# Performance work log

Hardware: AMD Instinct MI355X
Metric: run time of the kernel (lower is better)

## Reference

```python
import jax, jax.numpy as jnp
import numpy as np
from jax.ops import segment_sum

N, E, D, P, F_IN, L, G = 40000, 320000, 128, 16, 64, 3, 40


def setup_inputs():
    key = jax.random.key(0)
    ks = iter(jax.random.split(key, 64))
    nrm = lambda shape, s=0.1: s * jax.random.normal(next(ks), shape, jnp.float32)
    inp = {
        "node_feat": nrm((N, F_IN), 1.0),
        "pos_enc": nrm((N, P), 1.0),
        "edge_feat": nrm((E, 1), 1.0),
        "snorm_n": jnp.full((N, 1), 1.0 / np.sqrt(N / G), jnp.float32),
        "edge_src": jax.random.randint(next(ks), (E,), 0, N, jnp.int32),
        "edge_dst": jax.random.randint(next(ks), (E,), 0, N, jnp.int32),
        "batch_num_nodes": jnp.full((G,), N // G, jnp.int32),
        "W_h": nrm((F_IN, D)), "b_h": jnp.zeros((D,), jnp.float32),
        "W_p": nrm((P, D)), "b_p": jnp.zeros((D,), jnp.float32),
        "W_e": nrm((1, D)), "b_e": jnp.zeros((D,), jnp.float32),
        "A1_W": nrm((L, 2 * D, D)), "A1_b": jnp.zeros((L, D), jnp.float32),
        "A2_W": nrm((L, 2 * D, D)), "A2_b": jnp.zeros((L, D), jnp.float32),
        "B1_W": nrm((L, D, D)), "B1_b": jnp.zeros((L, D), jnp.float32),
        "B2_W": nrm((L, D, D)), "B2_b": jnp.zeros((L, D), jnp.float32),
        "B3_W": nrm((L, D, D)), "B3_b": jnp.zeros((L, D), jnp.float32),
        "C1_W": nrm((L, D, D)), "C1_b": jnp.zeros((L, D), jnp.float32),
        "C2_W": nrm((L, D, D)), "C2_b": jnp.zeros((L, D), jnp.float32),
        "bn_h_g": jnp.ones((L, D), jnp.float32), "bn_h_b": jnp.zeros((L, D), jnp.float32),
        "bn_e_g": jnp.ones((L, D), jnp.float32), "bn_e_b": jnp.zeros((L, D), jnp.float32),
        "pout_W": nrm((D, P)), "pout_b": jnp.zeros((P,), jnp.float32),
        "Whp_W": nrm((D + P, D)), "Whp_b": jnp.zeros((D,), jnp.float32),
        "mlp_W0": nrm((D, D // 2)), "mlp_b0": jnp.zeros((D // 2,), jnp.float32),
        "mlp_W1": nrm((D // 2, D // 4)), "mlp_b1": jnp.zeros((D // 4,), jnp.float32),
        "mlp_W2": nrm((D // 4, 1)), "mlp_b2": jnp.zeros((1,), jnp.float32),
    }
    return inp


def _bn(x, g, b, eps=1e-5):
    # BatchNorm1d with batch statistics (training-mode math, eval dropout)
    m = x.mean(0)
    v = x.var(0)
    return g * (x - m) / jnp.sqrt(v + eps) + b


def _forward(fl, edge_src, edge_dst, batch_num_nodes):
    n = fl["node_feat"].shape[0]
    h = fl["node_feat"] @ fl["W_h"] + fl["b_h"]
    p = fl["pos_enc"] @ fl["W_p"] + fl["b_p"]
    e = fl["edge_feat"] @ fl["W_e"] + fl["b_e"]
    snorm = fl["snorm_n"]
    for l in range(L):
        h_in, p_in, e_in = h, p, e
        hp_cat = jnp.concatenate([h, p], -1)                      # [N, 2D]
        A1h = hp_cat @ fl["A1_W"][l] + fl["A1_b"][l]
        A2h = hp_cat @ fl["A2_W"][l] + fl["A2_b"][l]
        B1h = h @ fl["B1_W"][l] + fl["B1_b"][l]
        B2h = h @ fl["B2_W"][l] + fl["B2_b"][l]
        B3e = e @ fl["B3_W"][l] + fl["B3_b"][l]
        hat_eta = B1h[edge_src] + B2h[edge_dst] + B3e             # [E, D]
        sigma = jax.nn.sigmoid(hat_eta)
        ssum = segment_sum(sigma, edge_dst, num_segments=n)       # [N, D]
        eta = sigma / (ssum[edge_dst] + 1e-6)                     # [E, D]
        h_new = A1h + segment_sum(eta * A2h[edge_src], edge_dst, num_segments=n)
        C1p = p @ fl["C1_W"][l] + fl["C1_b"][l]
        C2p = p @ fl["C2_W"][l] + fl["C2_b"][l]
        p_new = C1p + segment_sum(eta * C2p[edge_src], edge_dst, num_segments=n)
        h2 = jax.nn.relu(_bn(h_new * snorm, fl["bn_h_g"][l], fl["bn_h_b"][l]))
        e2 = jax.nn.relu(_bn(hat_eta, fl["bn_e_g"][l], fl["bn_e_b"][l]))
        p2 = jnp.tanh(p_new)
        h, p, e = h_in + h2, p_in + p2, e_in + e2                 # residual
    # LSPE readout: per-graph center and per-feature L2-normalize p
    p = p @ fl["pout_W"] + fl["pout_b"]                           # [N, P]
    gid = jnp.repeat(jnp.arange(G), batch_num_nodes, total_repeat_length=n)
    cnt = batch_num_nodes.astype(p.dtype)[:, None]
    p = p - (segment_sum(p, gid, num_segments=G) / cnt)[gid]
    p = p / jnp.sqrt(segment_sum(p * p, gid, num_segments=G))[gid]
    hp = jnp.concatenate([h, p], -1) @ fl["Whp_W"] + fl["Whp_b"]
    first_idx = jnp.concatenate([jnp.zeros((1,), jnp.int32),
                                 jnp.cumsum(batch_num_nodes)[:-1].astype(jnp.int32)])
    hg = hp[first_idx]                                            # [G, D]
    y = jax.nn.relu(hg @ fl["mlp_W0"] + fl["mlp_b0"])
    y = jax.nn.relu(y @ fl["mlp_W1"] + fl["mlp_b1"])
    return y @ fl["mlp_W2"] + fl["mlp_b2"]                        # [G, 1]


def reference(node_feat, pos_enc, edge_feat, snorm_n, edge_src, edge_dst,
              batch_num_nodes, W_h, b_h, W_p, b_p, W_e, b_e,
              A1_W, A1_b, A2_W, A2_b, B1_W, B1_b, B2_W, B2_b, B3_W, B3_b,
              C1_W, C1_b, C2_W, C2_b, bn_h_g, bn_h_b, bn_e_g, bn_e_b,
              pout_W, pout_b, Whp_W, Whp_b,
              mlp_W0, mlp_b0, mlp_W1, mlp_b1, mlp_W2, mlp_b2):
    args = dict(locals())
    src = args.pop("edge_src")
    dst = args.pop("edge_dst")
    bnn = args.pop("batch_num_nodes")
    return _forward(args, src, dst, bnn)
```

## Files before the change

### kernel.cpp

```cpp
#include <hip/hip_runtime.h>

#define NN 40000
#define NNP 40064
#define NE 320000
#define DD 128
#define PP 16
#define FIN 64
#define NL 3
#define NG 40

typedef float4 f4;
typedef __attribute__((ext_vector_type(4))) float f32x4;
typedef _Float16 hf;
typedef __attribute__((ext_vector_type(4))) _Float16 h4;
typedef __attribute__((ext_vector_type(8))) _Float16 h8;

__device__ hf    g_e   [NE * DD];
__device__ hf    g_heta[NE * DD];
__device__ float g_h   [NNP * DD], g_p [NNP * DD];
__device__ hf    g_h16 [NNP * DD], g_pf [NNP * DD];
__device__ float g_A1h [NNP * DD], g_C1p[NNP * DD];
__device__ hf    g_A2h [NNP * DD], g_B1h[NNP * DD], g_B2h[NNP * DD], g_C2p[NNP * DD];
__device__ float g_st  [768];
__device__ float g_p16 [NN * PP], g_psum[NG * PP], g_pss[NG * PP];
__device__ int   g_cum [64];
__device__ int   g_deg[NN], g_rowptr[NN + 1], g_cursor[NN], g_perm[NE], g_ssrc[NE], g_sdst[NE];
__device__ hf    g_WA[2 * NL * DD * 256];
__device__ hf    g_WB[5 * NL * DD * DD];

__device__ __forceinline__ float sigm(float x) { return 1.0f / (1.0f + __expf(-x)); }

__global__ void k_zero(float* __restrict__ p, int n4)
{
    int i = blockIdx.x * 256 + threadIdx.x;
    if (i < n4) ((f4*)p)[i] = f4{0.f, 0.f, 0.f, 0.f};
}

__global__ void k_zeroi(int* __restrict__ p, int n)
{
    int i = blockIdx.x * 256 + threadIdx.x;
    if (i < n) p[i] = 0;
}

__global__ void k_deg(const int* __restrict__ dst, int* __restrict__ deg)
{
    int e = blockIdx.x * 256 + threadIdx.x;
    if (e < NE) atomicAdd(&deg[dst[e]], 1);
}

__global__ __launch_bounds__(1024)
void k_scan(const int* __restrict__ deg, int* __restrict__ rowptr, int* __restrict__ cursor)
{
    __shared__ int sums[1024];
    int t = threadIdx.x;
    const int chunk = (NN + 1023) / 1024;
    int base = t * chunk;
    int s = 0;
    for (int i = 0; i < chunk; ++i) { int idx = base + i; if (idx < NN) s += deg[idx]; }
    sums[t] = s;
    __syncthreads();
    for (int off = 1; off < 1024; off <<= 1) {
        int v = (t >= off) ? sums[t - off] : 0;
        __syncthreads();
        sums[t] += v;
        __syncthreads();
    }
    int run = (t == 0) ? 0 : sums[t - 1];
    for (int i = 0; i < chunk; ++i) {
        int idx = base + i;
        if (idx < NN) { rowptr[idx] = run; cursor[idx] = run; run += deg[idx]; }
    }
    if (t == 1023) rowptr[NN] = sums[1023];
}

__global__ void k_fill(const int* __restrict__ dst, int* __restrict__ cursor,
                       int* __restrict__ perm)
{
    int e = blockIdx.x * 256 + threadIdx.x;
    if (e < NE) {
        int pos = atomicAdd(&cursor[dst[e]], 1);
        perm[pos] = e;
    }
}

__global__ void k_sortidx(const int* __restrict__ perm, const int* __restrict__ src,
                          const int* __restrict__ dst, int* __restrict__ ssrc,
                          int* __restrict__ sdst)
{
    int i = blockIdx.x * 256 + threadIdx.x;
    if (i < NE) { int e = perm[i]; ssrc[i] = src[e]; sdst[i] = dst[e]; }
}

__global__ void k_wprepA(const float* __restrict__ A1W, const float* __restrict__ A2W,
                         hf* __restrict__ outh)
{
    int which = blockIdx.z, l = blockIdx.y;
    int idx = blockIdx.x * 256 + threadIdx.x;
    int k = idx >> 7, n = idx & 127;
    const float* W = (which == 0 ? A1W : A2W) + (size_t)l * 256 * 128;
    outh[((size_t)which * NL + l) * DD * 256 + (size_t)n * 256 + k] = (hf)W[k * 128 + n];
}

__global__ void k_wprepB(const float* __restrict__ B1W, const float* __restrict__ B2W,
                         const float* __restrict__ B3W, const float* __restrict__ C1W,
                         const float* __restrict__ C2W, hf* __restrict__ outh)
{
    int which = blockIdx.z, l = blockIdx.y;
    int idx = blockIdx.x * 256 + threadIdx.x;
    int k = idx >> 7, n = idx & 127;
    const float* W;
    switch (which) { case 0: W = B1W; break; case 1: W = B2W; break;
                     case 2: W = B3W; break; case 3: W = C1W; break; default: W = C2W; }
    W += (size_t)l * 128 * 128;
    outh[((size_t)which * NL + l) * DD * DD + (size_t)n * 128 + k] = (hf)W[k * 128 + n];
}

template<int K>
__global__ __launch_bounds__(256)
void k_gemmF(const float* __restrict__ A, const float* __restrict__ W,
             const float* __restrict__ bias, float* __restrict__ C)
{
    __shared__ float As[64][20];
    __shared__ float Ws[16][128];
    const int tid = threadIdx.x;
    const int m0 = blockIdx.x * 64;
    const int ti = tid >> 4;
    const int tj = tid & 15;
    float acc[4][8];
    {
        float bv[8];
        #pragma unroll
        for (int c = 0; c < 8; ++c) bv[c] = bias[tj * 8 + c];
        #pragma unroll
        for (int r = 0; r < 4; ++r)
            #pragma unroll
            for (int c = 0; c < 8; ++c) acc[r][c] = bv[c];
    }
    const int ar = tid >> 2;
    const int ac = (tid & 3) * 4;
    for (int k0 = 0; k0 < K; k0 += 16) {
        f4 av = *(const f4*)(A + (size_t)(m0 + ar) * K + k0 + ac);
        *(f4*)&As[ar][ac] = av;
        {
            int q = tid;   int kr = q >> 5, c4 = (q & 31) * 4;
            *(f4*)&Ws[kr][c4] = *(const f4*)(W + (size_t)(k0 + kr) * 128 + c4);
            q = tid + 256; kr = q >> 5; c4 = (q & 31) * 4;
            *(f4*)&Ws[kr][c4] = *(const f4*)(W + (size_t)(k0 + kr) * 128 + c4);
        }
        __syncthreads();
        #pragma unroll
        for (int kk = 0; kk < 16; ++kk) {
            float a0 = As[ti * 4 + 0][kk];
            float a1 = As[ti * 4 + 1][kk];
            float a2 = As[ti * 4 + 2][kk];
            float a3 = As[ti * 4 + 3][kk];
            f4 w0 = *(f4*)&Ws[kk][tj * 8];
            f4 w1 = *(f4*)&Ws[kk][tj * 8 + 4];
            float wv[8] = {w0.x, w0.y, w0.z, w0.w, w1.x, w1.y, w1.z, w1.w};
            #pragma unroll
            for (int c = 0; c < 8; ++c) {
                acc[0][c] += a0 * wv[c];
                acc[1][c] += a1 * wv[c];
                acc[2][c] += a2 * wv[c];
                acc[3][c] += a3 * wv[c];
            }
        }
        __syncthreads();
    }
    #pragma unroll
    for (int r = 0; r < 4; ++r) {
        int row = m0 + ti * 4 + r;
        f4 o0 = {acc[r][0], acc[r][1], acc[r][2], acc[r][3]};
        f4 o1 = {acc[r][4], acc[r][5], acc[r][6], acc[r][7]};
        *(f4*)(C + (size_t)row * 128 + tj * 8)     = o0;
        *(f4*)(C + (size_t)row * 128 + tj * 8 + 4) = o1;
    }
}

struct NArgs {
    const hf* W[6];
    const float* bs[6];
    void* out[6];
};

__global__ __launch_bounds__(256)
void k_gemmN(NArgs a, const hf* __restrict__ hp, const hf* __restrict__ pp)
{
    __shared__ __align__(16) char smem[20480];
    hf (*As)[40] = (hf(*)[40])smem;
    hf (*Wh)[40] = (hf(*)[40])(smem + 10240);
    float* fstg = (float*)smem;
    hf*    hstg = (hf*)smem;
    const int tid = threadIdx.x;
    const int y = blockIdx.y;
    const int m0 = blockIdx.x * 128;
    const int K = (y < 2) ? 256 : 128;
    const hf* Wt = a.W[y];
    const int wid = tid >> 6, lane = tid & 63;
    const int lg = lane >> 4, ln = lane & 15;

    f32x4 acc[2][8];
    #pragma unroll
    for (int mt = 0; mt < 2; ++mt)
        #pragma unroll
        for (int nt = 0; nt < 8; ++nt) acc[mt][nt] = f32x4{0.f, 0.f, 0.f, 0.f};

    const int r1 = tid >> 2, g1 = (tid & 3) * 8;
    const int r2 = r1 + 64,  g2 = g1;

    for (int k0 = 0; k0 < K; k0 += 32) {
        const hf* pA; int kk;
        if (y < 2) {
            if (k0 >= 128) { pA = pp; kk = k0 - 128; }
            else           { pA = hp; kk = k0; }
        } else if (y < 4) { pA = hp; kk = k0; }
        else              { pA = pp; kk = k0; }
        *(f4*)&As[r1][g1] = *(const f4*)(pA + (size_t)(m0 + r1) * 128 + kk + g1);
        *(f4*)&As[r2][g2] = *(const f4*)(pA + (size_t)(m0 + r2) * 128 + kk + g2);
        *(f4*)&Wh[r1][g1] = *(const f4*)(Wt + (size_t)r1 * K + k0 + g1);
        *(f4*)&Wh[r2][g2] = *(const f4*)(Wt + (size_t)r2 * K + k0 + g2);
        __syncthreads();

        const int koff = lg * 8;
        h8 a0 = *(h8*)&As[wid * 32 + ln][koff];
        h8 a1 = *(h8*)&As[wid * 32 + 16 + ln][koff];
        #pragma unroll
        for (int nt = 0; nt < 8; ++nt) {
            h8 wh = *(h8*)&Wh[nt * 16 + ln][koff];
            acc[0][nt] = __builtin_amdgcn_mfma_f32_16x16x32_f16(a0, wh, acc[0][nt], 0, 0, 0);
            acc[1][nt] = __builtin_amdgcn_mfma_f32_16x16x32_f16(a1, wh, acc[1][nt], 0, 0, 0);
        }
        __syncthreads();
    }

    const float* bias = a.bs[y];
    const bool isF32 = (y == 0 || y == 4);
    if (isF32) {
        float* C = (float*)a.out[y];
        for (int pass = 0; pass < 4; ++pass) {
            if (wid == pass) {
                #pragma unroll
                for (int mt = 0; mt < 2; ++mt)
                    #pragma unroll
                    for (int nt = 0; nt < 8; ++nt)
                        #pragma unroll
                        for (int j = 0; j < 4; ++j)
                            fstg[(mt * 16 + lg * 4 + j) * 132 + nt * 16 + ln]
                                = acc[mt][nt][j] + bias[nt * 16 + ln];
            }
            __syncthreads();
            #pragma unroll
            for (int it = 0; it < 4; ++it) {
                int idx = it * 256 + tid;
                int r = idx >> 5, c4 = (idx & 31) * 4;
                *(f4*)(C + (size_t)(m0 + pass * 32 + r) * 128 + c4) = *(f4*)&fstg[r * 132 + c4];
            }
            __syncthreads();
        }
    } else {
        hf* C = (hf*)a.out[y];
        for (int pass = 0; pass < 4; ++pass) {
            if (wid == pass) {
                #pragma unroll
                for (int mt = 0; mt < 2; ++mt)
                    #pragma unroll
                    for (int nt = 0; nt < 8; ++nt)
                        #pragma unroll
                        for (int j = 0; j < 4; ++j)
                            hstg[(mt * 16 + lg * 4 + j) * 136 + nt * 16 + ln]
                                = (hf)(acc[mt][nt][j] + bias[nt * 16 + ln]);
            }
            __syncthreads();
            #pragma unroll
            for (int it = 0; it < 2; ++it) {
                int idx = it * 256 + tid;
                int r = idx >> 4, c8 = (idx & 15) * 8;
                *(f4*)(C + (size_t)(m0 + pass * 32 + r) * 128 + c8) = *(f4*)&hstg[r * 136 + c8];
            }
            __syncthreads();
        }
    }
}

template<bool EUPD, bool STATS>
__global__ __launch_bounds__(256)
void k_gemmE(hf* E, const hf* hetaPrev, hf* Cheta,
             const float* __restrict__ estPrev, const float* __restrict__ gamE,
             const float* __restrict__ betE,
             const hf* __restrict__ Wt,
             const float* __restrict__ bias,
             const hf* __restrict__ Gs, const hf* __restrict__ Gd,
             const int* __restrict__ srcI, const int* __restrict__ dstI,
             float* st, int wb)
{
    __shared__ __align__(16) char smem[20480];
    __shared__ float bnS[128], bnT[128];
    hf (*Ae)[40] = (hf(*)[40])smem;
    hf (*Wh)[40] = (hf(*)[40])(smem + 10240);
    float* sred = (float*)smem;
    hf*    hstg = (hf*)(smem + 1024);
    const int tid = threadIdx.x;
    const int m0 = blockIdx.x * 128;
    const int wid = tid >> 6, lane = tid & 63;
    const int lg = lane >> 4, ln = lane & 15;

    if (EUPD) {
        if (tid < 128) {
            const float invME = 1.0f / NE;
            float m = estPrev[tid] * invME;
            float v = estPrev[128 + tid] * invME - m * m;
            float inv = 1.0f / sqrtf(v + 1e-5f);
            float gg = gamE[tid];
            bnS[tid] = gg * inv;
            bnT[tid] = betE[tid] - gg * m * inv;
        }
        __syncthreads();
    }

    f32x4 acc[2][8];
    #pragma unroll
    for (int mt = 0; mt < 2; ++mt)
        #pragma unroll
        for (int nt = 0; nt < 8; ++nt) acc[mt][nt] = f32x4{0.f, 0.f, 0.f, 0.f};

    const int r1 = tid >> 2, g1 = (tid & 3) * 8;
    const int r2 = r1 + 64,  g2 = g1;

    for (int k0 = 0; k0 < 128; k0 += 32) {
        if (EUPD) {
            #pragma unroll
            for (int half = 0; half < 2; ++half) {
                int r = half ? r2 : r1;
                int g = half ? g2 : g1;
                int row = m0 + r, cb = k0 + g;
                h8 ev = *(const h8*)(E + (size_t)row * 128 + cb);
                h8 tv = *(const h8*)(hetaPrev + (size_t)row * 128 + cb);
                h8 nv;
                #pragma unroll
                for (int j = 0; j < 8; ++j) {
                    float xn = (float)tv[j] * bnS[cb + j] + bnT[cb + j];
                    float en = (float)ev[j] + fmaxf(xn, 0.f);
                    nv[j] = (hf)en;
                }
                *(h8*)&Ae[r][g] = nv;
                if (wb) *(h8*)(E + (size_t)row * 128 + cb) = nv;
            }
        } else {
            *(f4*)&Ae[r1][g1] = *(const f4*)(E + (size_t)(m0 + r1) * 128 + k0 + g1);
            *(f4*)&Ae[r2][g2] = *(const f4*)(E + (size_t)(m0 + r2) * 128 + k0 + g2);
        }
        *(f4*)&Wh[r1][g1] = *(const f4*)(Wt + (size_t)r1 * 128 + k0 + g1);
        *(f4*)&Wh[r2][g2] = *(const f4*)(Wt + (size_t)r2 * 128 + k0 + g2);
        __syncthreads();

        const int koff = lg * 8;
        h8 a0 = *(h8*)&Ae[wid * 32 + ln][koff];
        h8 a1 = *(h8*)&Ae[wid * 32 + 16 + ln][koff];
        #pragma unroll
        for (int nt = 0; nt < 8; ++nt) {
            h8 wh = *(h8*)&Wh[nt * 16 + ln][koff];
            acc[0][nt] = __builtin_amdgcn_mfma_f32_16x16x32_f16(a0, wh, acc[0][nt], 0, 0, 0);
            acc[1][nt] = __builtin_amdgcn_mfma_f32_16x16x32_f16(a1, wh, acc[1][nt], 0, 0, 0);
        }
        __syncthreads();
    }

    if (STATS) { sred[tid] = 0.f; __syncthreads(); }

    #pragma unroll
    for (int mt = 0; mt < 2; ++mt) {
        const int grow = m0 + wid * 32 + mt * 16 + lg * 4;
        int sa[4], da[4];
        #pragma unroll
        for (int j = 0; j < 4; ++j) { sa[j] = srcI[grow + j]; da[j] = dstI[grow + j]; }
        #pragma unroll
        for (int nt = 0; nt < 8; ++nt) {
            const int col = nt * 16 + ln;
            const float b = bias[col];
            float ls = 0.f, lq = 0.f;
            #pragma unroll
            for (int j = 0; j < 4; ++j) {
                float x = acc[mt][nt][j] + b
                        + (float)Gs[(size_t)sa[j] * 128 + col]
                        + (float)Gd[(size_t)da[j] * 128 + col];
                acc[mt][nt][j] = x;
                if (STATS) { ls += x; lq += x * x; }
            }
            if (STATS) {
                ls += __shfl_xor(ls, 16); ls += __shfl_xor(ls, 32);
                lq += __shfl_xor(lq, 16); lq += __shfl_xor(lq, 32);
                if (lane < 16) {
                    atomicAdd(&sred[col], ls);
                    atomicAdd(&sred[128 + col], lq);
                }
            }
        }
    }

    for (int pass = 0; pass < 4; ++pass) {
        if (wid == pass) {
            #pragma unroll
            for (int mt = 0; mt < 2; ++mt)
                #pragma unroll
                for (int nt = 0; nt < 8; ++nt)
                    #pragma unroll
                    for (int j = 0; j < 4; ++j)
                        hstg[(mt * 16 + lg * 4 + j) * 136 + nt * 16 + ln]
                            = (hf)acc[mt][nt][j];
        }
        __syncthreads();
        #pragma unroll
        for (int it = 0; it < 2; ++it) {
            int idx = it * 256 + tid;
            int r = idx >> 4, c8 = (idx & 15) * 8;
            *(f4*)(Cheta + (size_t)(m0 + pass * 32 + r) * 128 + c8) = *(f4*)&hstg[r * 136 + c8];
        }
        __syncthreads();
    }
    if (STATS) atomicAdd(&st[tid], sred[tid]);
}


__global__ void k_cvt16(const float* __restrict__ x, hf* __restrict__ y, int n4)
{
    int i = blockIdx.x * 256 + threadIdx.x;
    if (i >= n4) return;
    f4 v = ((const f4*)x)[i];
    ((h4*)y)[i] = h4{(hf)v.x, (hf)v.y, (hf)v.z, (hf)v.w};
}

__global__ void k_einit(const float* __restrict__ ef, const int* __restrict__ perm,
                        const float* __restrict__ We, const float* __restrict__ be,
                        hf* __restrict__ E)
{
    size_t id = (size_t)blockIdx.x * 256 + threadIdx.x;
    int row = (int)(id >> 5);
    int c = (int)(id & 31) * 4;
    float s = ef[perm[row]];
    f4 w = *(const f4*)(We + c);
    f4 b = *(const f4*)(be + c);
    *(h4*)(E + (size_t)row * 128 + c)
        = h4{(hf)(s * w.x + b.x), (hf)(s * w.y + b.y), (hf)(s * w.z + b.z), (hf)(s * w.w + b.w)};
}

__global__ void k_agg(const hf* __restrict__ heta, const hf* __restrict__ A2h,
                      const hf* __restrict__ C2p, const int* __restrict__ rowptr,
                      const int* __restrict__ ssrc, const float* __restrict__ snorm,
                      float* __restrict__ A1h, const float* __restrict__ C1p,
                      float* __restrict__ p, hf* __restrict__ pf,
                      float* __restrict__ st, int wp)
{
    size_t id = (size_t)blockIdx.x * 256 + threadIdx.x;
    int row = (int)(id >> 5);
    int c = (int)(id & 31) * 4;
    int s0 = rowptr[row], s1 = rowptr[row + 1];

    f4 ss = {0.f, 0.f, 0.f, 0.f};
    f4 ah = {0.f, 0.f, 0.f, 0.f};
    f4 cp = {0.f, 0.f, 0.f, 0.f};
    for (int e = s0; e < s1; ++e) {
        h4 v = *(const h4*)(heta + (size_t)e * 128 + c);
        int s = ssrc[e];
        h4 a = *(const h4*)(A2h + (size_t)s * 128 + c);
        h4 cc = *(const h4*)(C2p + (size_t)s * 128 + c);
        float g0 = sigm((float)v[0]), g1 = sigm((float)v[1]);
        float g2 = sigm((float)v[2]), g3 = sigm((float)v[3]);
        ss.x += g0; ss.y += g1; ss.z += g2; ss.w += g3;
        ah.x += g0 * (float)a[0]; ah.y += g1 * (float)a[1];
        ah.z += g2 * (float)a[2]; ah.w += g3 * (float)a[3];
        cp.x += g0 * (float)cc[0]; cp.y += g1 * (float)cc[1];
        cp.z += g2 * (float)cc[2]; cp.w += g3 * (float)cc[3];
    }
    ss.x += 1e-6f; ss.y += 1e-6f; ss.z += 1e-6f; ss.w += 1e-6f;
    ah.x /= ss.x; ah.y /= ss.y; ah.z /= ss.z; ah.w /= ss.w;
    cp.x /= ss.x; cp.y /= ss.y; cp.z /= ss.z; cp.w /= ss.w;

    float sn = snorm[row];
    f4 a1 = *(const f4*)(A1h + (size_t)row * 128 + c);
    f4 hx = {(a1.x + ah.x) * sn, (a1.y + ah.y) * sn, (a1.z + ah.z) * sn, (a1.w + ah.w) * sn};
    *(f4*)(A1h + (size_t)row * 128 + c) = hx;

    f4 c1 = *(const f4*)(C1p + (size_t)row * 128 + c);
    f4 pv = *(const f4*)(p + (size_t)row * 128 + c);
    pv.x += tanhf(c1.x + cp.x);
    pv.y += tanhf(c1.y + cp.y);
    pv.z += tanhf(c1.z + cp.z);
    pv.w += tanhf(c1.w + cp.w);
    *(f4*)(p + (size_t)row * 128 + c) = pv;
    if (wp)
        *(h4*)(pf + (size_t)row * 128 + c) = h4{(hf)pv.x, (hf)pv.y, (hf)pv.z, (hf)pv.w};

    __shared__ float red[8][128];
    int lrow = threadIdx.x >> 5;
    red[lrow][c + 0] = hx.x; red[lrow][c + 1] = hx.y;
    red[lrow][c + 2] = hx.z; red[lrow][c + 3] = hx.w;
    __syncthreads();
    if (threadIdx.x < 128) {
        float a = 0.f;
        #pragma unroll
        for (int q = 0; q < 8; ++q) a += red[q][threadIdx.x];
        atomicAdd(&st[threadIdx.x], a);
    }
    __syncthreads();
    red[lrow][c + 0] = hx.x * hx.x; red[lrow][c + 1] = hx.y * hx.y;
    red[lrow][c + 2] = hx.z * hx.z; red[lrow][c + 3] = hx.w * hx.w;
    __syncthreads();
    if (threadIdx.x < 128) {
        float a = 0.f;
        #pragma unroll
        for (int q = 0; q < 8; ++q) a += red[q][threadIdx.x];
        atomicAdd(&st[128 + threadIdx.x], a);
    }
}

__global__ void k_bnupd_h(float* __restrict__ Y, hf* __restrict__ Y16,
                          const float* __restrict__ X, const float* __restrict__ st,
                          const float* __restrict__ gam, const float* __restrict__ bet, float invM)
{
    size_t id = (size_t)blockIdx.x * 256 + threadIdx.x;
    int row = (int)(id >> 5);
    int c = (int)(id & 31) * 4;
    f4 x  = *(const f4*)(X + (size_t)row * 128 + c);
    f4 s  = *(const f4*)(st + c);
    f4 s2 = *(const f4*)(st + 128 + c);
    f4 g  = *(const f4*)(gam + c);
    f4 b  = *(const f4*)(bet + c);
    f4 y  = *(const f4*)(Y + (size_t)row * 128 + c);
    float m, v, o;
    m = s.x * invM; v = s2.x * invM - m * m; o = g.x * (x.x - m) / sqrtf(v + 1e-5f) + b.x; y.x += fmaxf(o, 0.f);
    m = s.y * invM; v = s2.y * invM - m * m; o = g.y * (x.y - m) / sqrtf(v + 1e-5f) + b.y; y.y += fmaxf(o, 0.f);
    m = s.z * invM; v = s2.z * invM - m * m; o = g.z * (x.z - m) / sqrtf(v + 1e-5f) + b.z; y.z += fmaxf(o, 0.f);
    m = s.w * invM; v = s2.w * invM - m * m; o = g.w * (x.w - m) / sqrtf(v + 1e-5f) + b.w; y.w += fmaxf(o, 0.f);
    *(f4*)(Y + (size_t)row * 128 + c) = y;
    *(h4*)(Y16 + (size_t)row * 128 + c) = h4{(hf)y.x, (hf)y.y, (hf)y.z, (hf)y.w};
}


__global__ void k_p16(const float* __restrict__ p, const float* __restrict__ poutW,
                      const float* __restrict__ poutb, float* __restrict__ p16)
{
    int id = blockIdx.x * 256 + threadIdx.x;
    int i = id >> 4, c = id & 15;
    float a = poutb[c];
    for (int k = 0; k < 128; ++k) a += p[(size_t)i * 128 + k] * poutW[k * 16 + c];
    p16[id] = a;
}

__global__ void k_cum(const int* __restrict__ bnn, int* __restrict__ cum)
{
    if (threadIdx.x == 0) {
        cum[0] = 0;
        for (int g = 0; g < NG; ++g) cum[g + 1] = cum[g] + bnn[g];
    }
}

__global__ void k_graphstats(const float* __restrict__ p16, const int* __restrict__ cum,
                             float* __restrict__ psum, float* __restrict__ pss)
{
    int g = blockIdx.x;
    int t = threadIdx.x;
    int c = t & 15, s = t >> 4;
    int start = cum[g], end = cum[g + 1];
    float cnt = (float)(end - start);
    __shared__ float red[16][17];
    __shared__ float meanv[16];
    float loc = 0.f;
    for (int i = start + s; i < end; i += 16) loc += p16[(size_t)i * 16 + c];
    red[s][c] = loc;
    __syncthreads();
    if (s == 0) {
        float a = 0.f;
        #pragma unroll
        for (int q = 0; q < 16; ++q) a += red[q][c];
        psum[g * 16 + c] = a;
        meanv[c] = a / cnt;
    }
    __syncthreads();
    float m = meanv[c];
    loc = 0.f;
    for (int i = start + s; i < end; i += 16) {
        float v = p16[(size_t)i * 16 + c] - m;
        loc += v * v;
    }
    red[s][c] = loc;
    __syncthreads();
    if (s == 0) {
        float a = 0.f;
        #pragma unroll
        for (int q = 0; q < 16; ++q) a += red[q][c];
        pss[g * 16 + c] = a;
    }
}

__global__ void k_final(const float* __restrict__ h, const float* __restrict__ A1h,
                        const float* __restrict__ hst, const float* __restrict__ gam,
                        const float* __restrict__ bet,
                        const float* __restrict__ p16,
                        const float* __restrict__ psum, const float* __restrict__ pss,
                        const int* __restrict__ cum,
                        const float* __restrict__ WhpW, const float* __restrict__ Whpb,
                        const float* __restrict__ W0, const float* __restrict__ b0,
                        const float* __restrict__ W1, const float* __restrict__ b1,
                        const float* __restrict__ W2, const float* __restrict__ b2,
                        float* __restrict__ out)
{
    int g = blockIdx.x;
    int t = threadIdx.x;
    __shared__ float hpc[144];
    __shared__ float hpv[128];
    __shared__ float y0[64];
    __shared__ float y1[32];
    int fi = cum[g];
    float cnt = (float)(cum[g + 1] - cum[g]);
    {
        const float invM = 1.0f / NN;
        float m = hst[t] * invM;
        float v = hst[128 + t] * invM - m * m;
        float x = A1h[(size_t)fi * 128 + t];
        float o = gam[t] * (x - m) / sqrtf(v + 1e-5f) + bet[t];
        hpc[t] = h[(size_t)fi * 128 + t] + fmaxf(o, 0.f);
    }
    if (t < 16) {
        float centered = p16[(size_t)fi * 16 + t] - psum[g * 16 + t] / cnt;
        hpc[128 + t] = centered / sqrtf(pss[g * 16 + t]);
    }
    __syncthreads();
    float acc = Whpb[t];
    for (int k = 0; k < 144; ++k) acc += hpc[k] * WhpW[k * 128 + t];
    hpv[t] = acc;
    __syncthreads();
    if (t < 64) {
        float a = b0[t];
        for (int k = 0; k < 128; ++k) a += hpv[k] * W0[k * 64 + t];
        y0[t] = fmaxf(a, 0.f);
    }
    __syncthreads();
    if (t < 32) {
        float a = b1[t];
        for (int k = 0; k < 64; ++k) a += y0[k] * W1[k * 32 + t];
        y1[t] = fmaxf(a, 0.f);
    }
    __syncthreads();
    if (t == 0) {
        float a = b2[0];
        for (int k = 0; k < 32; ++k) a += y1[k] * W2[k];
        out[g] = a;
    }
}


extern "C" void kernel_launch(void* const* d_in, const int* in_sizes, int n_in,
                              void* d_out, int out_size, void* d_ws, size_t ws_size,
                              hipStream_t stream)
{
    (void)in_sizes; (void)n_in; (void)out_size; (void)d_ws; (void)ws_size;
    const float* node_feat = (const float*)d_in[0];
    const float* pos_enc   = (const float*)d_in[1];
    const float* edge_feat = (const float*)d_in[2];
    const float* snorm     = (const float*)d_in[3];
    const int*   src       = (const int*)d_in[4];
    const int*   dst       = (const int*)d_in[5];
    const int*   bnn       = (const int*)d_in[6];
    const float* W_h = (const float*)d_in[7],  *b_h = (const float*)d_in[8];
    const float* W_p = (const float*)d_in[9],  *b_p = (const float*)d_in[10];
    const float* W_e = (const float*)d_in[11], *b_e = (const float*)d_in[12];
    const float* A1W = (const float*)d_in[13], *A1b = (const float*)d_in[14];
    const float* A2W = (const float*)d_in[15], *A2b = (const float*)d_in[16];
    const float* B1W = (const float*)d_in[17], *B1b = (const float*)d_in[18];
    const float* B2W = (const float*)d_in[19], *B2b = (const float*)d_in[20];
    const float* B3W = (const float*)d_in[21], *B3b = (const float*)d_in[22];
    const float* C1W = (const float*)d_in[23], *C1b = (const float*)d_in[24];
    const float* C2W = (const float*)d_in[25], *C2b = (const float*)d_in[26];
    const float* bnhg = (const float*)d_in[27], *bnhb = (const float*)d_in[28];
    const float* bneg = (const float*)d_in[29], *bneb = (const float*)d_in[30];
    const float* poutW = (const float*)d_in[31], *poutb = (const float*)d_in[32];
    const float* WhpW = (const float*)d_in[33], *Whpb = (const float*)d_in[34];
    const float* W0 = (const float*)d_in[35], *b0 = (const float*)d_in[36];
    const float* W1 = (const float*)d_in[37], *b1 = (const float*)d_in[38];
    const float* W2 = (const float*)d_in[39], *b2 = (const float*)d_in[40];
    float* out = (float*)d_out;

    float *h, *p, *A1h, *C1p, *st, *p16, *psum, *pss;
    hf *e, *heta, *h16, *pf, *A2h, *B1h, *B2h, *C2p, *WA, *WB;
    int *cum, *deg, *rowptr, *cursor, *perm, *ssrc, *sdst;
    hipGetSymbolAddress((void**)&e,      HIP_SYMBOL(g_e));
    hipGetSymbolAddress((void**)&heta,   HIP_SYMBOL(g_heta));
    hipGetSymbolAddress((void**)&h,      HIP_SYMBOL(g_h));
    hipGetSymbolAddress((void**)&p,      HIP_SYMBOL(g_p));
    hipGetSymbolAddress((void**)&h16,    HIP_SYMBOL(g_h16));
    hipGetSymbolAddress((void**)&pf,     HIP_SYMBOL(g_pf));
    hipGetSymbolAddress((void**)&A1h,    HIP_SYMBOL(g_A1h));
    hipGetSymbolAddress((void**)&C1p,    HIP_SYMBOL(g_C1p));
    hipGetSymbolAddress((void**)&A2h,    HIP_SYMBOL(g_A2h));
    hipGetSymbolAddress((void**)&B1h,    HIP_SYMBOL(g_B1h));
    hipGetSymbolAddress((void**)&B2h,    HIP_SYMBOL(g_B2h));
    hipGetSymbolAddress((void**)&C2p,    HIP_SYMBOL(g_C2p));
    hipGetSymbolAddress((void**)&st,     HIP_SYMBOL(g_st));
    hipGetSymbolAddress((void**)&p16,    HIP_SYMBOL(g_p16));
    hipGetSymbolAddress((void**)&psum,   HIP_SYMBOL(g_psum));
    hipGetSymbolAddress((void**)&pss,    HIP_SYMBOL(g_pss));
    hipGetSymbolAddress((void**)&cum,    HIP_SYMBOL(g_cum));
    hipGetSymbolAddress((void**)&deg,    HIP_SYMBOL(g_deg));
    hipGetSymbolAddress((void**)&rowptr, HIP_SYMBOL(g_rowptr));
    hipGetSymbolAddress((void**)&cursor, HIP_SYMBOL(g_cursor));
    hipGetSymbolAddress((void**)&perm,   HIP_SYMBOL(g_perm));
    hipGetSymbolAddress((void**)&ssrc,   HIP_SYMBOL(g_ssrc));
    hipGetSymbolAddress((void**)&sdst,   HIP_SYMBOL(g_sdst));
    hipGetSymbolAddress((void**)&WA,     HIP_SYMBOL(g_WA));
    hipGetSymbolAddress((void**)&WB,     HIP_SYMBOL(g_WB));
    float* hst  = st;
    float* estA = st + 256;
    float* estB = st + 512;

    k_zeroi<<<(NN + 255) / 256, 256, 0, stream>>>(deg, NN);
    k_deg<<<(NE + 255) / 256, 256, 0, stream>>>(dst, deg);
    k_scan<<<1, 1024, 0, stream>>>(deg, rowptr, cursor);
    k_fill<<<(NE + 255) / 256, 256, 0, stream>>>(dst, cursor, perm);
    k_sortidx<<<(NE + 255) / 256, 256, 0, stream>>>(perm, src, dst, ssrc, sdst);
    k_wprepA<<<dim3(128, NL, 2), 256, 0, stream>>>(A1W, A2W, WA);
    k_wprepB<<<dim3(64, NL, 5), 256, 0, stream>>>(B1W, B2W, B3W, C1W, C2W, WB);

    k_gemmF<FIN><<<NN / 64, 256, 0, stream>>>(node_feat, W_h, b_h, h);
    k_gemmF<PP ><<<NN / 64, 256, 0, stream>>>(pos_enc,  W_p, b_p, p);
    k_cvt16<<<(NNP * 32 + 255) / 256, 256, 0, stream>>>(h, h16, NNP * 32);
    k_cvt16<<<(NNP * 32 + 255) / 256, 256, 0, stream>>>(p, pf, NNP * 32);
    k_einit<<<NE * 32 / 256, 256, 0, stream>>>(edge_feat, perm, W_e, b_e, e);

    const int NB = NNP / 128;
    for (int l = 0; l < NL; ++l) {
        const hf* WB3 = WB + (size_t)(2 * NL + l) * DD * DD;

        NArgs na;
        na.W[0] = WA + (size_t)(0 * NL + l) * DD * 256;
        na.W[1] = WA + (size_t)(1 * NL + l) * DD * 256;
        na.W[2] = WB + (size_t)(0 * NL + l) * DD * DD;
        na.W[3] = WB + (size_t)(1 * NL + l) * DD * DD;
        na.W[4] = WB + (size_t)(3 * NL + l) * DD * DD;
        na.W[5] = WB + (size_t)(4 * NL + l) * DD * DD;
        na.bs[0] = A1b + l * DD; na.bs[1] = A2b + l * DD;
        na.bs[2] = B1b + l * DD; na.bs[3] = B2b + l * DD;
        na.bs[4] = C1b + l * DD; na.bs[5] = C2b + l * DD;
        na.out[0] = A1h; na.out[1] = A2h; na.out[2] = B1h;
        na.out[3] = B2h; na.out[4] = C1p; na.out[5] = C2p;
        k_gemmN<<<dim3(NB, 6), 256, 0, stream>>>(na, h16, pf);

        k_zero<<<1, 256, 0, stream>>>(hst, 64);

        if (l == 0) {
            k_zero<<<1, 256, 0, stream>>>(estA, 64);
            k_gemmE<false, true><<<NE / 128, 256, 0, stream>>>(
                e, nullptr, heta, nullptr, nullptr, nullptr,
                WB3, B3b + l * DD, B1h, B2h, ssrc, sdst, estA, 0);
        } else if (l == 1) {
            k_zero<<<1, 256, 0, stream>>>(estB, 64);
            k_gemmE<true, true><<<NE / 128, 256, 0, stream>>>(
                e, heta, heta, estA, bneg + 0 * DD, bneb + 0 * DD,
                WB3, B3b + l * DD, B1h, B2h, ssrc, sdst, estB, 1);
        } else {
            k_gemmE<true, false><<<NE / 128, 256, 0, stream>>>(
                e, heta, heta, estB, bneg + 1 * DD, bneb + 1 * DD,
                WB3, B3b + l * DD, B1h, B2h, ssrc, sdst, nullptr, 0);
        }

        k_agg<<<NN * 32 / 256, 256, 0, stream>>>(heta, A2h, C2p, rowptr, ssrc, snorm,
                                                 A1h, C1p, p, pf, hst,
                                                 (l < NL - 1) ? 1 : 0);

        if (l < NL - 1)
            k_bnupd_h<<<NN * 32 / 256, 256, 0, stream>>>(h, h16, A1h, hst,
                                                         bnhg + l * DD, bnhb + l * DD, 1.0f / NN);
    }

    k_p16<<<NN * 16 / 256, 256, 0, stream>>>(p, poutW, poutb, p16);
    k_cum<<<1, 64, 0, stream>>>(bnn, cum);
    k_graphstats<<<NG, 256, 0, stream>>>(p16, cum, psum, pss);
    k_final<<<NG, 128, 0, stream>>>(h, A1h, hst, bnhg + (NL - 1) * DD, bnhb + (NL - 1) * DD,
                                    p16, psum, pss, cum,
                                    WhpW, Whpb, W0, b0, W1, b1, W2, b2, out);
}
```

Baseline: 1.228 ms.

## Fold B1/B2 node projections into edge GEMM via concatenated gathered input

Removes the separate node-level B1/B2 GEMM outputs and instead has the edge GEMM multiply a K=384 concatenation of edge features, gathered h[src] and gathered h[dst] against stacked B3/B1/B2 weights, with summed biases. This eliminates writing and scattered element-wise gathering of B1h/B2h in the epilogue in favor of coalesced row gathers during the A-tile load. The trade-off is roughly tripling the edge GEMM's matrix work, recomputing projections per edge rather than per node.

```diff
diff --git a/kernel.cpp b/kernel.cpp
--- a/kernel.cpp
+++ b/kernel.cpp
@@ -20,13 +20,14 @@
 __device__ float g_h   [NNP * DD], g_p [NNP * DD];
 __device__ hf    g_h16 [NNP * DD], g_pf [NNP * DD];
 __device__ float g_A1h [NNP * DD], g_C1p[NNP * DD];
-__device__ hf    g_A2h [NNP * DD], g_B1h[NNP * DD], g_B2h[NNP * DD], g_C2p[NNP * DD];
-__device__ float g_st  [768];
+__device__ hf    g_A2h [NNP * DD], g_C2p[NNP * DD];
+__device__ float g_st  [896];
 __device__ float g_p16 [NN * PP], g_psum[NG * PP], g_pss[NG * PP];
 __device__ int   g_cum [64];
 __device__ int   g_deg[NN], g_rowptr[NN + 1], g_cursor[NN], g_perm[NE], g_ssrc[NE], g_sdst[NE];
 __device__ hf    g_WA[2 * NL * DD * 256];
-__device__ hf    g_WB[5 * NL * DD * DD];
+__device__ hf    g_WC[2 * NL * DD * DD];
+__device__ hf    g_WE[NL * DD * 384];
 
 __device__ __forceinline__ float sigm(float x) { return 1.0f / (1.0f + __expf(-x)); }
 
@@ -40,6 +41,13 @@
 {
     int i = blockIdx.x * 256 + threadIdx.x;
     if (i < n) p[i] = 0;
+}
+
+__global__ void k_ebias(const float* __restrict__ B1b, const float* __restrict__ B2b,
+                        const float* __restrict__ B3b, int l, float* __restrict__ outb)
+{
+    int t = threadIdx.x;
+    if (t < 128) outb[t] = B1b[l * 128 + t] + B2b[l * 128 + t] + B3b[l * 128 + t];
 }
 
 __global__ void k_deg(const int* __restrict__ dst, int* __restrict__ deg)
@@ -101,18 +109,29 @@
     outh[((size_t)which * NL + l) * DD * 256 + (size_t)n * 256 + k] = (hf)W[k * 128 + n];
 }
 
-__global__ void k_wprepB(const float* __restrict__ B1W, const float* __restrict__ B2W,
-                         const float* __restrict__ B3W, const float* __restrict__ C1W,
-                         const float* __restrict__ C2W, hf* __restrict__ outh)
+__global__ void k_wprepC(const float* __restrict__ C1W, const float* __restrict__ C2W,
+                         hf* __restrict__ outh)
 {
     int which = blockIdx.z, l = blockIdx.y;
     int idx = blockIdx.x * 256 + threadIdx.x;
     int k = idx >> 7, n = idx & 127;
+    const float* W = (which == 0 ? C1W : C2W) + (size_t)l * 128 * 128;
+    outh[((size_t)which * NL + l) * DD * DD + (size_t)n * 128 + k] = (hf)W[k * 128 + n];
+}
+
+__global__ void k_wprepE(const float* __restrict__ B1W, const float* __restrict__ B2W,
+                         const float* __restrict__ B3W, hf* __restrict__ outh)
+{
+    int l = blockIdx.y;
+    int idx = blockIdx.x * 256 + threadIdx.x;
+    int k = idx >> 7, n = idx & 127;
     const float* W;
-    switch (which) { case 0: W = B1W; break; case 1: W = B2W; break;
-                     case 2: W = B3W; break; case 3: W = C1W; break; default: W = C2W; }
+    int kk;
+    if (k < 128)      { W = B3W; kk = k; }
+    else if (k < 256) { W = B1W; kk = k - 128; }
+    else              { W = B2W; kk = k - 256; }
     W += (size_t)l * 128 * 128;
-    outh[((size_t)which * NL + l) * DD * DD + (size_t)n * 128 + k] = (hf)W[k * 128 + n];
+    outh[(size_t)l * DD * 384 + (size_t)n * 384 + k] = (hf)W[kk * 128 + n];
 }
 
 template<int K>
@@ -178,9 +197,9 @@
 }
 
 struct NArgs {
-    const hf* W[6];
-    const float* bs[6];
-    void* out[6];
+    const hf* W[4];
+    const float* bs[4];
+    void* out[4];
 };
 
 __global__ __launch_bounds__(256)
@@ -213,8 +232,7 @@
         if (y < 2) {
             if (k0 >= 128) { pA = pp; kk = k0 - 128; }
             else           { pA = hp; kk = k0; }
-        } else if (y < 4) { pA = hp; kk = k0; }
-        else              { pA = pp; kk = k0; }
+        } else { pA = pp; kk = k0; }
         *(f4*)&As[r1][g1] = *(const f4*)(pA + (size_t)(m0 + r1) * 128 + kk + g1);
         *(f4*)&As[r2][g2] = *(const f4*)(pA + (size_t)(m0 + r2) * 128 + kk + g2);
         *(f4*)&Wh[r1][g1] = *(const f4*)(Wt + (size_t)r1 * K + k0 + g1);
@@ -234,7 +252,7 @@
     }
 
     const float* bias = a.bs[y];
-    const bool isF32 = (y == 0 || y == 4);
+    const bool isF32 = (y == 0 || y == 2);
     if (isF32) {
         float* C = (float*)a.out[y];
         for (int pass = 0; pass < 4; ++pass) {
@@ -289,7 +307,7 @@
              const float* __restrict__ betE,
              const hf* __restrict__ Wt,
              const float* __restrict__ bias,
-             const hf* __restrict__ Gs, const hf* __restrict__ Gd,
+             const hf* __restrict__ h16,
              const int* __restrict__ srcI, const int* __restrict__ dstI,
              float* st, int wb)
 {
@@ -325,32 +343,44 @@
 
     const int r1 = tid >> 2, g1 = (tid & 3) * 8;
     const int r2 = r1 + 64,  g2 = g1;
-
-    for (int k0 = 0; k0 < 128; k0 += 32) {
-        if (EUPD) {
-            #pragma unroll
-            for (int half = 0; half < 2; ++half) {
-                int r = half ? r2 : r1;
-                int g = half ? g2 : g1;
-                int row = m0 + r, cb = k0 + g;
-                h8 ev = *(const h8*)(E + (size_t)row * 128 + cb);
-                h8 tv = *(const h8*)(hetaPrev + (size_t)row * 128 + cb);
-                h8 nv;
+    const int s1 = srcI[m0 + r1], s2 = srcI[m0 + r2];
+    const int d1 = dstI[m0 + r1], d2 = dstI[m0 + r2];
+
+    for (int k0 = 0; k0 < 384; k0 += 32) {
+        if (k0 < 128) {
+            if (EUPD) {
                 #pragma unroll
-                for (int j = 0; j < 8; ++j) {
-                    float xn = (float)tv[j] * bnS[cb + j] + bnT[cb + j];
-                    float en = (float)ev[j] + fmaxf(xn, 0.f);
-                    nv[j] = (hf)en;
+                for (int half = 0; half < 2; ++half) {
+                    int r = half ? r2 : r1;
+                    int g = half ? g2 : g1;
+                    int row = m0 + r, cb = k0 + g;
+                    h8 ev = *(const h8*)(E + (size_t)row * 128 + cb);
+                    h8 tv = *(const h8*)(hetaPrev + (size_t)row * 128 + cb);
+                    h8 nv;
+                    #pragma unroll
+                    for (int j = 0; j < 8; ++j) {
+                        float xn = (float)tv[j] * bnS[cb + j] + bnT[cb + j];
+                        float en = (float)ev[j] + fmaxf(xn, 0.f);
+                        nv[j] = (hf)en;
+                    }
+                    *(h8*)&Ae[r][g] = nv;
+                    if (wb) *(h8*)(E + (size_t)row * 128 + cb) = nv;
                 }
-                *(h8*)&Ae[r][g] = nv;
-                if (wb) *(h8*)(E + (size_t)row * 128 + cb) = nv;
+            } else {
+                *(f4*)&Ae[r1][g1] = *(const f4*)(E + (size_t)(m0 + r1) * 128 + k0 + g1);
+                *(f4*)&Ae[r2][g2] = *(const f4*)(E + (size_t)(m0 + r2) * 128 + k0 + g2);
             }
+        } else if (k0 < 256) {
+            int kk = k0 - 128;
+            *(f4*)&Ae[r1][g1] = *(const f4*)(h16 + (size_t)s1 * 128 + kk + g1);
+            *(f4*)&Ae[r2][g2] = *(const f4*)(h16 + (size_t)s2 * 128 + kk + g2);
         } else {
-            *(f4*)&Ae[r1][g1] = *(const f4*)(E + (size_t)(m0 + r1) * 128 + k0 + g1);
-            *(f4*)&Ae[r2][g2] = *(const f4*)(E + (size_t)(m0 + r2) * 128 + k0 + g2);
-        }
-        *(f4*)&Wh[r1][g1] = *(const f4*)(Wt + (size_t)r1 * 128 + k0 + g1);
-        *(f4*)&Wh[r2][g2] = *(const f4*)(Wt + (size_t)r2 * 128 + k0 + g2);
+            int kk = k0 - 256;
+            *(f4*)&Ae[r1][g1] = *(const f4*)(h16 + (size_t)d1 * 128 + kk + g1);
+            *(f4*)&Ae[r2][g2] = *(const f4*)(h16 + (size_t)d2 * 128 + kk + g2);
+        }
+        *(f4*)&Wh[r1][g1] = *(const f4*)(Wt + (size_t)r1 * 384 + k0 + g1);
+        *(f4*)&Wh[r2][g2] = *(const f4*)(Wt + (size_t)r2 * 384 + k0 + g2);
         __syncthreads();
 
         const int koff = lg * 8;
@@ -369,10 +399,6 @@
 
     #pragma unroll
     for (int mt = 0; mt < 2; ++mt) {
-        const int grow = m0 + wid * 32 + mt * 16 + lg * 4;
-        int sa[4], da[4];
-        #pragma unroll
-        for (int j = 0; j < 4; ++j) { sa[j] = srcI[grow + j]; da[j] = dstI[grow + j]; }
         #pragma unroll
         for (int nt = 0; nt < 8; ++nt) {
             const int col = nt * 16 + ln;
@@ -380,9 +406,7 @@
             float ls = 0.f, lq = 0.f;
             #pragma unroll
             for (int j = 0; j < 4; ++j) {
-                float x = acc[mt][nt][j] + b
-                        + (float)Gs[(size_t)sa[j] * 128 + col]
-                        + (float)Gd[(size_t)da[j] * 128 + col];
+                float x = acc[mt][nt][j] + b;
                 acc[mt][nt][j] = x;
                 if (STATS) { ls += x; lq += x * x; }
             }
@@ -681,7 +705,7 @@
     float* out = (float*)d_out;
 
     float *h, *p, *A1h, *C1p, *st, *p16, *psum, *pss;
-    hf *e, *heta, *h16, *pf, *A2h, *B1h, *B2h, *C2p, *WA, *WB;
+    hf *e, *heta, *h16, *pf, *A2h, *C2p, *WA, *WC, *WE;
     int *cum, *deg, *rowptr, *cursor, *perm, *ssrc, *sdst;
     hipGetSymbolAddress((void**)&e,      HIP_SYMBOL(g_e));
     hipGetSymbolAddress((void**)&heta,   HIP_SYMBOL(g_heta));
@@ -692,8 +716,6 @@
     hipGetSymbolAddress((void**)&A1h,    HIP_SYMBOL(g_A1h));
     hipGetSymbolAddress((void**)&C1p,    HIP_SYMBOL(g_C1p));
     hipGetSymbolAddress((void**)&A2h,    HIP_SYMBOL(g_A2h));
-    hipGetSymbolAddress((void**)&B1h,    HIP_SYMBOL(g_B1h));
-    hipGetSymbolAddress((void**)&B2h,    HIP_SYMBOL(g_B2h));
     hipGetSymbolAddress((void**)&C2p,    HIP_SYMBOL(g_C2p));
     hipGetSymbolAddress((void**)&st,     HIP_SYMBOL(g_st));
     hipGetSymbolAddress((void**)&p16,    HIP_SYMBOL(g_p16));
@@ -707,10 +729,12 @@
     hipGetSymbolAddress((void**)&ssrc,   HIP_SYMBOL(g_ssrc));
     hipGetSymbolAddress((void**)&sdst,   HIP_SYMBOL(g_sdst));
     hipGetSymbolAddress((void**)&WA,     HIP_SYMBOL(g_WA));
-    hipGetSymbolAddress((void**)&WB,     HIP_SYMBOL(g_WB));
-    float* hst  = st;
-    float* estA = st + 256;
-    float* estB = st + 512;
+    hipGetSymbolAddress((void**)&WC,     HIP_SYMBOL(g_WC));
+    hipGetSymbolAddress((void**)&WE,     HIP_SYMBOL(g_WE));
+    float* hst   = st;
+    float* estA  = st + 256;
+    float* estB  = st + 512;
+    float* ebias = st + 768;
 
     k_zeroi<<<(NN + 255) / 256, 256, 0, stream>>>(deg, NN);
     k_deg<<<(NE + 255) / 256, 256, 0, stream>>>(dst, deg);
@@ -718,7 +742,8 @@
     k_fill<<<(NE + 255) / 256, 256, 0, stream>>>(dst, cursor, perm);
     k_sortidx<<<(NE + 255) / 256, 256, 0, stream>>>(perm, src, dst, ssrc, sdst);
     k_wprepA<<<dim3(128, NL, 2), 256, 0, stream>>>(A1W, A2W, WA);
-    k_wprepB<<<dim3(64, NL, 5), 256, 0, stream>>>(B1W, B2W, B3W, C1W, C2W, WB);
+    k_wprepC<<<dim3(64, NL, 2), 256, 0, stream>>>(C1W, C2W, WC);
+    k_wprepE<<<dim3(192, NL), 256, 0, stream>>>(B1W, B2W, B3W, WE);
 
     k_gemmF<FIN><<<NN / 64, 256, 0, stream>>>(node_feat, W_h, b_h, h);
     k_gemmF<PP ><<<NN / 64, 256, 0, stream>>>(pos_enc,  W_p, b_p, p);
@@ -728,38 +753,35 @@
 
     const int NB = NNP / 128;
     for (int l = 0; l < NL; ++l) {
-        const hf* WB3 = WB + (size_t)(2 * NL + l) * DD * DD;
+        const hf* WEl = WE + (size_t)l * DD * 384;
 
         NArgs na;
         na.W[0] = WA + (size_t)(0 * NL + l) * DD * 256;
         na.W[1] = WA + (size_t)(1 * NL + l) * DD * 256;
-        na.W[2] = WB + (size_t)(0 * NL + l) * DD * DD;
-        na.W[3] = WB + (size_t)(1 * NL + l) * DD * DD;
-        na.W[4] = WB + (size_t)(3 * NL + l) * DD * DD;
-        na.W[5] = WB + (size_t)(4 * NL + l) * DD * DD;
+        na.W[2] = WC + (size_t)(0 * NL + l) * DD * DD;
+        na.W[3] = WC + (size_t)(1 * NL + l) * DD * DD;
         na.bs[0] = A1b + l * DD; na.bs[1] = A2b + l * DD;
-        na.bs[2] = B1b + l * DD; na.bs[3] = B2b + l * DD;
-        na.bs[4] = C1b + l * DD; na.bs[5] = C2b + l * DD;
-        na.out[0] = A1h; na.out[1] = A2h; na.out[2] = B1h;
-        na.out[3] = B2h; na.out[4] = C1p; na.out[5] = C2p;
-        k_gemmN<<<dim3(NB, 6), 256, 0, stream>>>(na, h16, pf);
+        na.bs[2] = C1b + l * DD; na.bs[3] = C2b + l * DD;
+        na.out[0] = A1h; na.out[1] = A2h; na.out[2] = C1p; na.out[3] = C2p;
+        k_gemmN<<<dim3(NB, 4), 256, 0, stream>>>(na, h16, pf);
 
         k_zero<<<1, 256, 0, stream>>>(hst, 64);
+        k_ebias<<<1, 128, 0, stream>>>(B1b, B2b, B3b, l, ebias);
 
         if (l == 0) {
             k_zero<<<1, 256, 0, stream>>>(estA, 64);
             k_gemmE<false, true><<<NE / 128, 256, 0, stream>>>(
                 e, nullptr, heta, nullptr, nullptr, nullptr,
-                WB3, B3b + l * DD, B1h, B2h, ssrc, sdst, estA, 0);
+                WEl, ebias, h16, ssrc, sdst, estA, 0);
         } else if (l == 1) {
             k_zero<<<1, 256, 0, stream>>>(estB, 64);
             k_gemmE<true, true><<<NE / 128, 256, 0, stream>>>(
                 e, heta, heta, estA, bneg + 0 * DD, bneb + 0 * DD,
-                WB3, B3b + l * DD, B1h, B2h, ssrc, sdst, estB, 1);
+                WEl, ebias, h16, ssrc, sdst, estB, 1);
         } else {
             k_gemmE<true, false><<<NE / 128, 256, 0, stream>>>(
                 e, heta, heta, estB, bneg + 1 * DD, bneb + 1 * DD,
-                WB3, B3b + l * DD, B1h, B2h, ssrc, sdst, nullptr, 0);
+                WEl, ebias, h16, ssrc, sdst, nullptr, 0);
         }
 
         k_agg<<<NN * 32 / 256, 256, 0, stream>>>(heta, A2h, C2p, rowptr, ssrc, snorm,
```

Result: slower. 1.271 ms (+3.6%).

## Double-buffer LDS tiles in node and edge MFMA GEMM kernels

Applied to the files above, without the earlier changes.

Restructures the K-loop of both the node GEMM and the edge GEMM to use two LDS buffers. The next k-slice is staged while the current one feeds the MFMAs, which drops one barrier per iteration. The LDS row pitch also shrinks from 40 to 36 halves. In exchange, per-block LDS grows from 20 KB to 36 KB, which can lower occupancy. The new pitch breaks 16-byte alignment of the 128-bit LDS accesses and may change bank-conflict behaviour.

```diff
diff --git a/kernel.cpp b/kernel.cpp
--- a/kernel.cpp
+++ b/kernel.cpp
@@ -177,6 +177,9 @@
     }
 }
 
+#define TP 36
+#define TSZ 9216
+
 struct NArgs {
     const hf* W[6];
     const float* bs[6];
@@ -186,9 +189,7 @@
 __global__ __launch_bounds__(256)
 void k_gemmN(NArgs a, const hf* __restrict__ hp, const hf* __restrict__ pp)
 {
-    __shared__ __align__(16) char smem[20480];
-    hf (*As)[40] = (hf(*)[40])smem;
-    hf (*Wh)[40] = (hf(*)[40])(smem + 10240);
+    __shared__ __align__(16) char smem[36864];
     float* fstg = (float*)smem;
     hf*    hstg = (hf*)smem;
     const int tid = threadIdx.x;
@@ -206,9 +207,11 @@
         for (int nt = 0; nt < 8; ++nt) acc[mt][nt] = f32x4{0.f, 0.f, 0.f, 0.f};
 
     const int r1 = tid >> 2, g1 = (tid & 3) * 8;
-    const int r2 = r1 + 64,  g2 = g1;
-
-    for (int k0 = 0; k0 < K; k0 += 32) {
+    const int r2 = r1 + 64;
+
+    auto stage = [&](int k0, int b) {
+        hf (*As)[TP] = (hf(*)[TP])(smem + b * TSZ);
+        hf (*Ws)[TP] = (hf(*)[TP])(smem + 18432 + b * TSZ);
         const hf* pA; int kk;
         if (y < 2) {
             if (k0 >= 128) { pA = pp; kk = k0 - 128; }
@@ -216,20 +219,30 @@
         } else if (y < 4) { pA = hp; kk = k0; }
         else              { pA = pp; kk = k0; }
         *(f4*)&As[r1][g1] = *(const f4*)(pA + (size_t)(m0 + r1) * 128 + kk + g1);
-        *(f4*)&As[r2][g2] = *(const f4*)(pA + (size_t)(m0 + r2) * 128 + kk + g2);
-        *(f4*)&Wh[r1][g1] = *(const f4*)(Wt + (size_t)r1 * K + k0 + g1);
-        *(f4*)&Wh[r2][g2] = *(const f4*)(Wt + (size_t)r2 * K + k0 + g2);
-        __syncthreads();
-
+        *(f4*)&As[r2][g1] = *(const f4*)(pA + (size_t)(m0 + r2) * 128 + kk + g1);
+        *(f4*)&Ws[r1][g1] = *(const f4*)(Wt + (size_t)r1 * K + k0 + g1);
+        *(f4*)&Ws[r2][g1] = *(const f4*)(Wt + (size_t)r2 * K + k0 + g1);
+    };
+    auto compute = [&](int b) {
+        hf (*As)[TP] = (hf(*)[TP])(smem + b * TSZ);
+        hf (*Ws)[TP] = (hf(*)[TP])(smem + 18432 + b * TSZ);
         const int koff = lg * 8;
         h8 a0 = *(h8*)&As[wid * 32 + ln][koff];
         h8 a1 = *(h8*)&As[wid * 32 + 16 + ln][koff];
         #pragma unroll
         for (int nt = 0; nt < 8; ++nt) {
-            h8 wh = *(h8*)&Wh[nt * 16 + ln][koff];
+            h8 wh = *(h8*)&Ws[nt * 16 + ln][koff];
             acc[0][nt] = __builtin_amdgcn_mfma_f32_16x16x32_f16(a0, wh, acc[0][nt], 0, 0, 0);
             acc[1][nt] = __builtin_amdgcn_mfma_f32_16x16x32_f16(a1, wh, acc[1][nt], 0, 0, 0);
         }
+    };
+
+    stage(0, 0);
+    __syncthreads();
+    const int nIt = K / 32;
+    for (int i = 0; i < nIt; ++i) {
+        if (i + 1 < nIt) stage((i + 1) * 32, (i + 1) & 1);
+        compute(i & 1);
         __syncthreads();
     }
 
@@ -293,10 +306,8 @@
              const int* __restrict__ srcI, const int* __restrict__ dstI,
              float* st, int wb)
 {
-    __shared__ __align__(16) char smem[20480];
+    __shared__ __align__(16) char smem[36864];
     __shared__ float bnS[128], bnT[128];
-    hf (*Ae)[40] = (hf(*)[40])smem;
-    hf (*Wh)[40] = (hf(*)[40])(smem + 10240);
     float* sred = (float*)smem;
     hf*    hstg = (hf*)(smem + 1024);
     const int tid = threadIdx.x;
@@ -324,15 +335,16 @@
         for (int nt = 0; nt < 8; ++nt) acc[mt][nt] = f32x4{0.f, 0.f, 0.f, 0.f};
 
     const int r1 = tid >> 2, g1 = (tid & 3) * 8;
-    const int r2 = r1 + 64,  g2 = g1;
-
-    for (int k0 = 0; k0 < 128; k0 += 32) {
+    const int r2 = r1 + 64;
+
+    auto stage = [&](int k0, int b) {
+        hf (*Ae)[TP] = (hf(*)[TP])(smem + b * TSZ);
+        hf (*Ws)[TP] = (hf(*)[TP])(smem + 18432 + b * TSZ);
         if (EUPD) {
             #pragma unroll
             for (int half = 0; half < 2; ++half) {
                 int r = half ? r2 : r1;
-                int g = half ? g2 : g1;
-                int row = m0 + r, cb = k0 + g;
+                int row = m0 + r, cb = k0 + g1;
                 h8 ev = *(const h8*)(E + (size_t)row * 128 + cb);
                 h8 tv = *(const h8*)(hetaPrev + (size_t)row * 128 + cb);
                 h8 nv;
@@ -342,26 +354,35 @@
                     float en = (float)ev[j] + fmaxf(xn, 0.f);
                     nv[j] = (hf)en;
                 }
-                *(h8*)&Ae[r][g] = nv;
+                *(h8*)&Ae[r][g1] = nv;
                 if (wb) *(h8*)(E + (size_t)row * 128 + cb) = nv;
             }
         } else {
             *(f4*)&Ae[r1][g1] = *(const f4*)(E + (size_t)(m0 + r1) * 128 + k0 + g1);
-            *(f4*)&Ae[r2][g2] = *(const f4*)(E + (size_t)(m0 + r2) * 128 + k0 + g2);
-        }
-        *(f4*)&Wh[r1][g1] = *(const f4*)(Wt + (size_t)r1 * 128 + k0 + g1);
-        *(f4*)&Wh[r2][g2] = *(const f4*)(Wt + (size_t)r2 * 128 + k0 + g2);
-        __syncthreads();
-
+            *(f4*)&Ae[r2][g1] = *(const f4*)(E + (size_t)(m0 + r2) * 128 + k0 + g1);
+        }
+        *(f4*)&Ws[r1][g1] = *(const f4*)(Wt + (size_t)r1 * 128 + k0 + g1);
+        *(f4*)&Ws[r2][g1] = *(const f4*)(Wt + (size_t)r2 * 128 + k0 + g1);
+    };
+    auto compute = [&](int b) {
+        hf (*Ae)[TP] = (hf(*)[TP])(smem + b * TSZ);
+        hf (*Ws)[TP] = (hf(*)[TP])(smem + 18432 + b * TSZ);
         const int koff = lg * 8;
         h8 a0 = *(h8*)&Ae[wid * 32 + ln][koff];
         h8 a1 = *(h8*)&Ae[wid * 32 + 16 + ln][koff];
         #pragma unroll
         for (int nt = 0; nt < 8; ++nt) {
-            h8 wh = *(h8*)&Wh[nt * 16 + ln][koff];
+            h8 wh = *(h8*)&Ws[nt * 16 + ln][koff];
             acc[0][nt] = __builtin_amdgcn_mfma_f32_16x16x32_f16(a0, wh, acc[0][nt], 0, 0, 0);
             acc[1][nt] = __builtin_amdgcn_mfma_f32_16x16x32_f16(a1, wh, acc[1][nt], 0, 0, 0);
         }
+    };
+
+    stage(0, 0);
+    __syncthreads();
+    for (int i = 0; i < 4; ++i) {
+        if (i + 1 < 4) stage((i + 1) * 32, (i + 1) & 1);
+        compute(i & 1);
         __syncthreads();
     }
 
```

After: 1.670 ms. +36.1%, slower.
